# Optimization experiments

Measured on AMD Instinct MI355X. Metric: run time of the kernel, lower is better.

## Reference

```python
import jax, jax.numpy as jnp
import numpy as np

DIM = 1024
HEADS = 16
HEAD_DIM = DIM // HEADS
HIDDEN = 4 * DIM
B, N = 2, 2048
LS_INIT = 1e-4


def _layernorm(x, w, b, eps=1e-5):
    mu = jnp.mean(x, axis=-1, keepdims=True)
    var = jnp.var(x, axis=-1, keepdims=True)
    return (x - mu) * jax.lax.rsqrt(var + eps) * w + b


def setup_inputs() -> dict:
    key = jax.random.key(0)
    ks = jax.random.split(key, 8)
    s = 0.02
    return {
        "x": jax.random.normal(ks[0], (B, N, DIM), jnp.float32),
        "ln1_w": jnp.ones((DIM,), jnp.float32),
        "ln1_b": jnp.zeros((DIM,), jnp.float32),
        "qkv_w": jax.random.normal(ks[1], (3 * DIM, DIM), jnp.float32) * s,
        "qkv_b": jnp.zeros((3 * DIM,), jnp.float32),
        "proj_w": jax.random.normal(ks[2], (DIM, DIM), jnp.float32) * s,
        "proj_b": jnp.zeros((DIM,), jnp.float32),
        "ls1_gamma": jnp.full((DIM,), LS_INIT, jnp.float32),
        "ln2_w": jnp.ones((DIM,), jnp.float32),
        "ln2_b": jnp.zeros((DIM,), jnp.float32),
        "fc1_w": jax.random.normal(ks[3], (HIDDEN, DIM), jnp.float32) * s,
        "fc1_b": jnp.zeros((HIDDEN,), jnp.float32),
        "fc2_w": jax.random.normal(ks[4], (DIM, HIDDEN), jnp.float32) * s,
        "fc2_b": jnp.zeros((DIM,), jnp.float32),
        "ls2_gamma": jnp.full((DIM,), LS_INIT, jnp.float32),
    }


def reference(x, ln1_w, ln1_b, qkv_w, qkv_b, proj_w, proj_b, ls1_gamma,
              ln2_w, ln2_b, fc1_w, fc1_b, fc2_w, fc2_b, ls2_gamma):
    Bn, Nn, C = x.shape
    scale = HEAD_DIM ** -0.5

    # --- attention branch (pre-norm) ---
    h = _layernorm(x, ln1_w, ln1_b)
    qkv = h @ qkv_w.T + qkv_b                      # [B,N,3C]
    qkv = qkv.reshape(Bn, Nn, 3, HEADS, HEAD_DIM)
    q = qkv[:, :, 0].transpose(0, 2, 1, 3)         # [B,H,N,D]
    k = qkv[:, :, 1].transpose(0, 2, 1, 3)
    v = qkv[:, :, 2].transpose(0, 2, 1, 3)
    attn = jnp.einsum('bhnd,bhmd->bhnm', q, k) * scale  # [B,H,N,N]
    attn = jax.nn.softmax(attn, axis=-1)
    o = jnp.einsum('bhnm,bhmd->bhnd', attn, v)
    o = o.transpose(0, 2, 1, 3).reshape(Bn, Nn, C)
    o = o @ proj_w.T + proj_b
    x = x + o * ls1_gamma

    # --- MLP branch (pre-norm) ---
    h = _layernorm(x, ln2_w, ln2_b)
    h = jax.nn.gelu(h @ fc1_w.T + fc1_b, approximate=False)
    h = h @ fc2_w.T + fc2_b
    x = x + h * ls2_gamma
    return x
```

## Files before the change

### kernel.cpp

```cpp
#include <hip/hip_runtime.h>

#define DIM 1024
#define HEADS 16
#define HEAD_DIM 64
#define HIDDEN 4096
#define BB 2
#define NN 2048
#define TOK (BB*NN)

typedef __attribute__((ext_vector_type(8))) short bf16x8;
typedef __attribute__((ext_vector_type(4))) float f32x4;
typedef __attribute__((ext_vector_type(2))) int i32x2;

__device__ inline short f2bf(float f) {
    unsigned u = __float_as_uint(f);
    unsigned r = (u + 0x7fff + ((u >> 16) & 1)) >> 16;
    return (short)r;
}

#define GLL16(g, l)                                                          \
    __builtin_amdgcn_global_load_lds(                                        \
        (const __attribute__((address_space(1))) void*)(g),                  \
        (__attribute__((address_space(3))) void*)(l), 16, 0, 0)

#define BARRIER() do { asm volatile("" ::: "memory");                        \
    __builtin_amdgcn_s_barrier();                                            \
    asm volatile("" ::: "memory"); } while (0)

__global__ void cvt_kernel(const float* __restrict__ in, short* __restrict__ out, int n4) {
    int i = blockIdx.x * blockDim.x + threadIdx.x;
    int stride = gridDim.x * blockDim.x;
    for (; i < n4; i += stride) {
        float4 v = ((const float4*)in)[i];
        short4 o;
        o.x = f2bf(v.x); o.y = f2bf(v.y); o.z = f2bf(v.z); o.w = f2bf(v.w);
        ((short4*)out)[i] = o;
    }
}

__global__ __launch_bounds__(256) void ln_kernel(const float* __restrict__ x,
                                                 const float* __restrict__ w,
                                                 const float* __restrict__ b,
                                                 short* __restrict__ out) {
    const int row = blockIdx.x;
    const int t = threadIdx.x;
    float4 v = ((const float4*)(x + (long)row * DIM))[t];
    float s = v.x + v.y + v.z + v.w;
    float ss = v.x * v.x + v.y * v.y + v.z * v.z + v.w * v.w;
#pragma unroll
    for (int m = 1; m < 64; m <<= 1) {
        s += __shfl_xor(s, m);
        ss += __shfl_xor(ss, m);
    }
    __shared__ float rs[4], rss[4];
    int wv = t >> 6;
    if ((t & 63) == 0) { rs[wv] = s; rss[wv] = ss; }
    __syncthreads();
    s = rs[0] + rs[1] + rs[2] + rs[3];
    ss = rss[0] + rss[1] + rss[2] + rss[3];
    float mean = s * (1.f / DIM);
    float var = ss * (1.f / DIM) - mean * mean;
    float rstd = rsqrtf(var + 1e-5f);
    float4 wv4 = ((const float4*)w)[t];
    float4 bv4 = ((const float4*)b)[t];
    short4 o;
    o.x = f2bf((v.x - mean) * rstd * wv4.x + bv4.x);
    o.y = f2bf((v.y - mean) * rstd * wv4.y + bv4.y);
    o.z = f2bf((v.z - mean) * rstd * wv4.z + bv4.z);
    o.w = f2bf((v.w - mean) * rstd * wv4.w + bv4.w);
    ((short4*)(out + (long)row * DIM))[t] = o;
}

template <int EPI, int BM>
__global__ __launch_bounds__(512, 2) void gemm8(const short* __restrict__ A,
                                                const short* __restrict__ Bt,
                                                const float* __restrict__ bias,
                                                const float* __restrict__ resid,
                                                const float* __restrict__ gamma,
                                                void* __restrict__ Cout,
                                                int M, int N, int K, int nbx) {
    constexpr int ALOADS = BM / 64;
    constexpr int MMP = BM / 64;
    constexpr int AR = BM / 32;

    __shared__ __align__(16) short As[2][BM * 64];
    __shared__ __align__(16) short Bs[2][2][128 * 64];

    const int t = threadIdx.x;
    const int w = t >> 6, l = t & 63, lr = l & 15, lg = l >> 4;
    const int wr = w >> 2, wc = w & 3;

    const int nwg = gridDim.x;
    const int id = blockIdx.x;
    const int r = (id & 7) * (nwg >> 3) + (id >> 3);
    const int by = r / nbx, bx = r % nbx;
    const int rowBase = by * BM, colBase = bx * 256;

    f32x4 acc[AR][4];
#pragma unroll
    for (int m = 0; m < AR; m++)
#pragma unroll
        for (int n = 0; n < 4; n++) acc[m][n] = {0.f, 0.f, 0.f, 0.f};

    bf16x8 afr[MMP][2];
    bf16x8 bfr[4][2];

    const int NT = K >> 6;
    const int ITERS = NT >> 1;

    auto stageA = [&](int buf, int tile) {
        const long k0 = (long)tile * 64;
#pragma unroll
        for (int j = 0; j < ALOADS; j++) {
            int L = j * 512 + t;
            int p = L >> 3;
            int colS = ((L & 7) ^ (p & 7)) << 3;
            const short* g = A + (long)(rowBase + p) * K + k0 + colS;
            GLL16(g, &As[buf][(j * 512 + w * 64) * 8]);
        }
    };
    auto stageBh = [&](int buf, int h, int tile) {
        const long k0 = (long)tile * 64;
#pragma unroll
        for (int j = 0; j < 2; j++) {
            int L = j * 512 + t;
            int p = L >> 3;
            int gcol = ((p >> 5) << 6) + (h << 5) + (p & 31);
            int colS = ((L & 7) ^ (p & 7)) << 3;
            const short* g = Bt + (long)(colBase + gcol) * K + k0 + colS;
            GLL16(g, &Bs[buf][h][(j * 512 + w * 64) * 8]);
        }
    };
    auto ldA = [&](int buf, int mh) {
#pragma unroll
        for (int mm = 0; mm < MMP; mm++) {
            int phys = wr * (BM / 2) + mh * (BM / 4) + mm * 16 + lr;
            int base = phys * 64, sw = (phys & 7) << 3;
#pragma unroll
            for (int ks = 0; ks < 2; ks++)
                afr[mm][ks] = *(const bf16x8*)&As[buf][base + ((ks * 32 + lg * 8) ^ sw)];
        }
    };
    auto ldB = [&](int buf, int nh) {
#pragma unroll
        for (int nn = 0; nn < 2; nn++) {
            int phys = wc * 32 + nn * 16 + lr;
            int base = phys * 64, sw = (phys & 7) << 3;
#pragma unroll
            for (int ks = 0; ks < 2; ks++)
                bfr[nh * 2 + nn][ks] = *(const bf16x8*)&Bs[buf][nh][base + ((ks * 32 + lg * 8) ^ sw)];
        }
    };
    auto mfmaQ = [&](int mh, int nh) {
        __builtin_amdgcn_s_setprio(1);
#pragma unroll
        for (int ks = 0; ks < 2; ks++)
#pragma unroll
            for (int mm = 0; mm < MMP; mm++)
#pragma unroll
                for (int nn = 0; nn < 2; nn++)
                    acc[mh * MMP + mm][nh * 2 + nn] = __builtin_amdgcn_mfma_f32_16x16x32_bf16(
                        afr[mm][ks], bfr[nh * 2 + nn][ks], acc[mh * MMP + mm][nh * 2 + nn], 0, 0, 0);
        __builtin_amdgcn_s_setprio(0);
    };
    auto waitVM = [&]() {
        if constexpr (BM == 256) asm volatile("s_waitcnt vmcnt(8)" ::: "memory");
        else                     asm volatile("s_waitcnt vmcnt(6)" ::: "memory");
    };

    stageBh(0, 0, 0); stageBh(0, 1, 0); stageA(0, 0);
    stageBh(1, 0, 1); stageBh(1, 1, 1); stageA(1, 1);
    waitVM();
    BARRIER();

    for (int i = 0; i < ITERS; i++) {
        const bool more = (i < ITERS - 1);
        ldA(0, 0); ldB(0, 0);
        BARRIER(); mfmaQ(0, 0); BARRIER();
        ldB(0, 1);
        if (more) stageBh(0, 0, 2 * i + 2);
        BARRIER(); mfmaQ(0, 1); BARRIER();
        ldA(0, 1);
        if (more) stageBh(0, 1, 2 * i + 2);
        BARRIER(); mfmaQ(1, 0); BARRIER();
        if (more) { stageA(0, 2 * i + 2); waitVM(); }
        else      { asm volatile("s_waitcnt vmcnt(0)" ::: "memory"); }
        BARRIER(); mfmaQ(1, 1); BARRIER();
        ldA(1, 0); ldB(1, 0);
        BARRIER(); mfmaQ(0, 0); BARRIER();
        ldB(1, 1);
        if (more) stageBh(1, 0, 2 * i + 3);
        BARRIER(); mfmaQ(0, 1); BARRIER();
        ldA(1, 1);
        if (more) stageBh(1, 1, 2 * i + 3);
        BARRIER(); mfmaQ(1, 0); BARRIER();
        if (more) { stageA(1, 2 * i + 3); waitVM(); }
        else      { asm volatile("s_waitcnt vmcnt(0)" ::: "memory"); }
        BARRIER(); mfmaQ(1, 1); BARRIER();
    }

#pragma unroll
    for (int n = 0; n < 4; n++) {
        int col = colBase + wc * 64 + n * 16 + lr;
        float bs = bias[col];
        float gm = (EPI == 3) ? gamma[col] : 0.f;
#pragma unroll
        for (int m = 0; m < AR; m++) {
            int row0 = rowBase + wr * (BM / 2) + m * 16 + lg * 4;
#pragma unroll
            for (int j = 0; j < 4; j++) {
                int row = row0 + j;
                float v = acc[m][n][j] + bs;
                if (EPI == 1) { if (col < DIM) v *= 0.125f; }
                if (EPI == 2) { v = 0.5f * v * (1.f + erff(v * 0.70710678118f)); }
                if (EPI == 3) {
                    float o = resid[(long)row * N + col] + v * gm;
                    ((float*)Cout)[(long)row * N + col] = o;
                } else {
                    ((short*)Cout)[(long)row * N + col] = f2bf(v);
                }
            }
        }
    }
}

__global__ __launch_bounds__(256) void attn_kernel(const short* __restrict__ qkv,
                                                   short* __restrict__ out) {
    const int id = blockIdx.x;
    const int rank = (id & 7) * 128 + (id >> 3);
    const int bh = rank >> 5, qt = rank & 31;
    const int b = bh >> 4, h = bh & 15;
    const int t = threadIdx.x;
    const int w = t >> 6, l = t & 63, lr = l & 15, lg = l >> 4;

    __shared__ __align__(16) short Ks[2][4096];
    __shared__ __align__(16) short Vs[2][4096];
    __shared__ __align__(16) short Ps[4][1024];

    bf16x8 qf[2];
    {
        const int qtok = b * NN + qt * 64 + w * 16 + lr;
        const short* qp = qkv + (long)qtok * (3 * DIM) + h * HEAD_DIM;
        qf[0] = *(const bf16x8*)(qp + lg * 8);
        qf[1] = *(const bf16x8*)(qp + 32 + lg * 8);
    }

    bf16x8 ones;
#pragma unroll
    for (int i = 0; i < 8; i++) ones[i] = (short)0x3F80;

    f32x4 o[4];
#pragma unroll
    for (int dn = 0; dn < 4; dn++) o[dn] = {0.f, 0.f, 0.f, 0.f};
    float mrow[4] = {-1e30f, -1e30f, -1e30f, -1e30f};
    float lrow[4] = {0.f, 0.f, 0.f, 0.f};

    const long tokbase = (long)(b * NN) * (3 * DIM);

    auto stage = [&](int cb, int kv0) {
#pragma unroll
        for (int r = 0; r < 2; r++) {
            int L = r * 256 + t;
            int krow = L >> 3;
            int kcol = ((L & 7) * 8) ^ ((krow & 7) << 3);
            const short* gk = qkv + tokbase + (long)(kv0 + krow) * (3 * DIM) + DIM + h * HEAD_DIM + kcol;
            GLL16(gk, &Ks[cb][(r * 256 + w * 64) * 8]);
            int kv = ((L >> 5) << 2) | ((L >> 1) & 3);
            int d  = ((L >> 3) & 3) * 16 + (L & 1) * 8;
            const short* gv = qkv + tokbase + (long)(kv0 + kv) * (3 * DIM) + 2 * DIM + h * HEAD_DIM + d;
            GLL16(gv, &Vs[cb][(r * 256 + w * 64) * 8]);
        }
    };

    stage(0, 0);
    int cur = 0;

    for (int kvt = 0; kvt < NN / 64; kvt++) {
        __syncthreads();
        if (kvt + 1 < NN / 64) stage(cur ^ 1, (kvt + 1) * 64);

        const int kswz = (lr & 7) << 3;
        f32x4 s[4];
#pragma unroll
        for (int n = 0; n < 4; n++) {
            int rowoff = (n * 16 + lr) * 64;
            bf16x8 kf0 = *(const bf16x8*)&Ks[cur][rowoff + ((lg * 8) ^ kswz)];
            bf16x8 kf1 = *(const bf16x8*)&Ks[cur][rowoff + ((32 + lg * 8) ^ kswz)];
            s[n] = {0.f, 0.f, 0.f, 0.f};
            s[n] = __builtin_amdgcn_mfma_f32_16x16x32_bf16(qf[0], kf0, s[n], 0, 0, 0);
            s[n] = __builtin_amdgcn_mfma_f32_16x16x32_bf16(qf[1], kf1, s[n], 0, 0, 0);
        }

        float corr[4];
#pragma unroll
        for (int j = 0; j < 4; j++) {
            float mx = fmaxf(fmaxf(s[0][j], s[1][j]), fmaxf(s[2][j], s[3][j]));
#pragma unroll
            for (int msk = 1; msk < 16; msk <<= 1) mx = fmaxf(mx, __shfl_xor(mx, msk));
            float mnew = fmaxf(mrow[j], mx);
            corr[j] = __expf(mrow[j] - mnew);
            mrow[j] = mnew;
            int prow = lg * 4 + j;
            int pswz = (prow & 7) << 3;
#pragma unroll
            for (int n = 0; n < 4; n++) {
                float p = __expf(s[n][j] - mnew);
                Ps[w][prow * 64 + ((n * 16 + lr) ^ pswz)] = f2bf(p);
            }
#pragma unroll
            for (int dn = 0; dn < 4; dn++) o[dn][j] *= corr[j];
        }

        i32x2 vrlo[2][4], vrhi[2][4];
#pragma unroll
        for (int kb = 0; kb < 2; kb++)
#pragma unroll
            for (int dn = 0; dn < 4; dn++) {
                unsigned voff = (unsigned)(size_t)&Vs[cur][(kb * 8 + lg * 2) * 256 + dn * 64 + lr];
                asm volatile("ds_read_b64_tr_b16 %0, %2\n\t"
                             "ds_read_b64_tr_b16 %1, %2 offset:512"
                             : "=&v"(vrlo[kb][dn]), "=&v"(vrhi[kb][dn])
                             : "v"(voff));
            }
        asm volatile("s_waitcnt lgkmcnt(0)" ::: "memory");
        __builtin_amdgcn_sched_barrier(0);

        f32x4 lsum = {0.f, 0.f, 0.f, 0.f};
#pragma unroll
        for (int kb = 0; kb < 2; kb++) {
            bf16x8 pf = *(const bf16x8*)&Ps[w][lr * 64 + ((kb * 32 + lg * 8) ^ ((lr & 7) << 3))];
            lsum = __builtin_amdgcn_mfma_f32_16x16x32_bf16(pf, ones, lsum, 0, 0, 0);
#pragma unroll
            for (int dn = 0; dn < 4; dn++) {
                union { i32x2 p[2]; bf16x8 v; } u;
                u.p[0] = vrlo[kb][dn];
                u.p[1] = vrhi[kb][dn];
                o[dn] = __builtin_amdgcn_mfma_f32_16x16x32_bf16(pf, u.v, o[dn], 0, 0, 0);
            }
        }
#pragma unroll
        for (int j = 0; j < 4; j++) lrow[j] = lrow[j] * corr[j] + lsum[j];

        cur ^= 1;
    }

#pragma unroll
    for (int j = 0; j < 4; j++) {
        float inv = 1.f / lrow[j];
        long tok = b * NN + qt * 64 + w * 16 + lg * 4 + j;
#pragma unroll
        for (int dn = 0; dn < 4; dn++)
            out[tok * DIM + h * HEAD_DIM + dn * 16 + lr] = f2bf(o[dn][j] * inv);
    }
}

extern "C" void kernel_launch(void* const* d_in, const int* in_sizes, int n_in,
                              void* d_out, int out_size, void* d_ws, size_t ws_size,
                              hipStream_t stream) {
    const float* x       = (const float*)d_in[0];
    const float* ln1_w   = (const float*)d_in[1];
    const float* ln1_b   = (const float*)d_in[2];
    const float* qkv_w   = (const float*)d_in[3];
    const float* qkv_b   = (const float*)d_in[4];
    const float* proj_w  = (const float*)d_in[5];
    const float* proj_b  = (const float*)d_in[6];
    const float* ls1_g   = (const float*)d_in[7];
    const float* ln2_w   = (const float*)d_in[8];
    const float* ln2_b   = (const float*)d_in[9];
    const float* fc1_w   = (const float*)d_in[10];
    const float* fc1_b   = (const float*)d_in[11];
    const float* fc2_w   = (const float*)d_in[12];
    const float* fc2_b   = (const float*)d_in[13];
    const float* ls2_g   = (const float*)d_in[14];

    char* p = (char*)d_ws;
    short* wqkv   = (short*)p; p += (size_t)3 * DIM * DIM * 2;
    short* wproj  = (short*)p; p += (size_t)DIM * DIM * 2;
    short* wfc1   = (short*)p; p += (size_t)HIDDEN * DIM * 2;
    short* wfc2   = (short*)p; p += (size_t)DIM * HIDDEN * 2;
    short* h1     = (short*)p; p += (size_t)TOK * DIM * 2;
    short* qkvbuf = (short*)p; p += (size_t)TOK * 3 * DIM * 2;
    short* attno  = (short*)p; p += (size_t)TOK * DIM * 2;
    float* x2     = (float*)p; p += (size_t)TOK * DIM * 4;
    short* h2     = (short*)p; p += (size_t)TOK * DIM * 2;
    short* fc1o   = (short*)p; p += (size_t)TOK * HIDDEN * 2;

    {
        int n4;
        n4 = 3 * DIM * DIM / 4;
        cvt_kernel<<<dim3(2048), dim3(256), 0, stream>>>(qkv_w, wqkv, n4);
        n4 = DIM * DIM / 4;
        cvt_kernel<<<dim3(1024), dim3(256), 0, stream>>>(proj_w, wproj, n4);
        n4 = HIDDEN * DIM / 4;
        cvt_kernel<<<dim3(2048), dim3(256), 0, stream>>>(fc1_w, wfc1, n4);
        n4 = DIM * HIDDEN / 4;
        cvt_kernel<<<dim3(2048), dim3(256), 0, stream>>>(fc2_w, wfc2, n4);
    }

    ln_kernel<<<dim3(TOK), dim3(256), 0, stream>>>(x, ln1_w, ln1_b, h1);

    gemm8<1, 256><<<dim3(192), dim3(512), 0, stream>>>(
        h1, wqkv, qkv_b, nullptr, nullptr, qkvbuf, TOK, 3 * DIM, DIM, 12);

    attn_kernel<<<dim3(NN / 64 * BB * HEADS), dim3(256), 0, stream>>>(qkvbuf, attno);

    gemm8<3, 128><<<dim3(128), dim3(512), 0, stream>>>(
        attno, wproj, proj_b, x, ls1_g, x2, TOK, DIM, DIM, 4);

    ln_kernel<<<dim3(TOK), dim3(256), 0, stream>>>(x2, ln2_w, ln2_b, h2);

    gemm8<2, 256><<<dim3(256), dim3(512), 0, stream>>>(
        h2, wfc1, fc1_b, nullptr, nullptr, fc1o, TOK, HIDDEN, DIM, 16);

    gemm8<3, 128><<<dim3(128), dim3(512), 0, stream>>>(
        fc1o, wfc2, fc2_b, x2, ls2_g, (float*)d_out, TOK, DIM, HIDDEN, 4);
}
```

Baseline: 442.8 us.

## Widen attention KV tile to 128 and add lazy softmax rescaling

Doubles the KV tile processed per iteration in the flash-attention kernel from 64 to 128 keys, halving the number of barriers and pipeline stages and enlarging the K/V/P shared buffers. It also skips the running-max update and output rescale unless some lane's new max exceeds the old one by more than 8, a lazy-rescale trick that keeps exp values bounded. V reads are interleaved per k-block rather than loaded all at once. This raises LDS use (about 80KB per block), which may reduce occupancy, and adds register pressure from the 8 score tiles.

```diff
diff --git a/kernel.cpp b/kernel.cpp
--- a/kernel.cpp
+++ b/kernel.cpp
@@ -233,9 +233,9 @@
     const int t = threadIdx.x;
     const int w = t >> 6, l = t & 63, lr = l & 15, lg = l >> 4;
 
-    __shared__ __align__(16) short Ks[2][4096];
-    __shared__ __align__(16) short Vs[2][4096];
-    __shared__ __align__(16) short Ps[4][1024];
+    __shared__ __align__(16) short Ks[2][128 * 64];
+    __shared__ __align__(16) short Vs[2][2 * 4096];
+    __shared__ __align__(16) short Ps[4][16 * 128];
 
     bf16x8 qf[2];
     {
@@ -259,30 +259,35 @@
 
     auto stage = [&](int cb, int kv0) {
 #pragma unroll
-        for (int r = 0; r < 2; r++) {
-            int L = r * 256 + t;
+        for (int j = 0; j < 4; j++) {
+            int L = j * 256 + t;
             int krow = L >> 3;
             int kcol = ((L & 7) * 8) ^ ((krow & 7) << 3);
             const short* gk = qkv + tokbase + (long)(kv0 + krow) * (3 * DIM) + DIM + h * HEAD_DIM + kcol;
-            GLL16(gk, &Ks[cb][(r * 256 + w * 64) * 8]);
-            int kv = ((L >> 5) << 2) | ((L >> 1) & 3);
-            int d  = ((L >> 3) & 3) * 16 + (L & 1) * 8;
-            const short* gv = qkv + tokbase + (long)(kv0 + kv) * (3 * DIM) + 2 * DIM + h * HEAD_DIM + d;
-            GLL16(gv, &Vs[cb][(r * 256 + w * 64) * 8]);
+            GLL16(gk, &Ks[cb][(j * 256 + w * 64) * 8]);
+        }
+#pragma unroll
+        for (int j = 0; j < 4; j++) {
+            int L = j * 256 + t;
+            int hf = L >> 9, Lh = L & 511;
+            int kvl = ((Lh >> 5) << 2) | ((Lh >> 1) & 3);
+            int d  = ((Lh >> 3) & 3) * 16 + (Lh & 1) * 8;
+            const short* gv = qkv + tokbase + (long)(kv0 + hf * 64 + kvl) * (3 * DIM) + 2 * DIM + h * HEAD_DIM + d;
+            GLL16(gv, &Vs[cb][(j * 256 + w * 64) * 8]);
         }
     };
 
     stage(0, 0);
     int cur = 0;
 
-    for (int kvt = 0; kvt < NN / 64; kvt++) {
+    for (int kvt = 0; kvt < NN / 128; kvt++) {
         __syncthreads();
-        if (kvt + 1 < NN / 64) stage(cur ^ 1, (kvt + 1) * 64);
+        if (kvt + 1 < NN / 128) stage(cur ^ 1, (kvt + 1) * 128);
 
         const int kswz = (lr & 7) << 3;
-        f32x4 s[4];
-#pragma unroll
-        for (int n = 0; n < 4; n++) {
+        f32x4 s[8];
+#pragma unroll
+        for (int n = 0; n < 8; n++) {
             int rowoff = (n * 16 + lr) * 64;
             bf16x8 kf0 = *(const bf16x8*)&Ks[cur][rowoff + ((lg * 8) ^ kswz)];
             bf16x8 kf1 = *(const bf16x8*)&Ks[cur][rowoff + ((32 + lg * 8) ^ kswz)];
@@ -294,47 +299,50 @@
         float corr[4];
 #pragma unroll
         for (int j = 0; j < 4; j++) {
-            float mx = fmaxf(fmaxf(s[0][j], s[1][j]), fmaxf(s[2][j], s[3][j]));
+            float mx = s[0][j];
+#pragma unroll
+            for (int n = 1; n < 8; n++) mx = fmaxf(mx, s[n][j]);
 #pragma unroll
             for (int msk = 1; msk < 16; msk <<= 1) mx = fmaxf(mx, __shfl_xor(mx, msk));
-            float mnew = fmaxf(mrow[j], mx);
-            corr[j] = __expf(mrow[j] - mnew);
-            mrow[j] = mnew;
+            corr[j] = 1.f;
+            if (!__all(mx - mrow[j] <= 8.f)) {
+                float mnew = fmaxf(mrow[j], mx);
+                corr[j] = __expf(mrow[j] - mnew);
+                mrow[j] = mnew;
+#pragma unroll
+                for (int dn = 0; dn < 4; dn++) o[dn][j] *= corr[j];
+            }
             int prow = lg * 4 + j;
             int pswz = (prow & 7) << 3;
 #pragma unroll
-            for (int n = 0; n < 4; n++) {
-                float p = __expf(s[n][j] - mnew);
-                Ps[w][prow * 64 + ((n * 16 + lr) ^ pswz)] = f2bf(p);
+            for (int n = 0; n < 8; n++) {
+                float p = __expf(s[n][j] - mrow[j]);
+                Ps[w][prow * 128 + ((n * 16 + lr) ^ pswz)] = f2bf(p);
             }
-#pragma unroll
-            for (int dn = 0; dn < 4; dn++) o[dn][j] *= corr[j];
-        }
-
-        i32x2 vrlo[2][4], vrhi[2][4];
-#pragma unroll
-        for (int kb = 0; kb < 2; kb++)
+        }
+
+        f32x4 lsum = {0.f, 0.f, 0.f, 0.f};
+#pragma unroll
+        for (int kb = 0; kb < 4; kb++) {
+            const int hf = kb >> 1, kb2 = kb & 1;
+            i32x2 vlo[4], vhi[4];
 #pragma unroll
             for (int dn = 0; dn < 4; dn++) {
-                unsigned voff = (unsigned)(size_t)&Vs[cur][(kb * 8 + lg * 2) * 256 + dn * 64 + lr];
+                unsigned voff = (unsigned)(size_t)&Vs[cur][hf * 4096 + (kb2 * 8 + lg * 2) * 256 + dn * 64 + lr];
                 asm volatile("ds_read_b64_tr_b16 %0, %2\n\t"
                              "ds_read_b64_tr_b16 %1, %2 offset:512"
-                             : "=&v"(vrlo[kb][dn]), "=&v"(vrhi[kb][dn])
+                             : "=&v"(vlo[dn]), "=&v"(vhi[dn])
                              : "v"(voff));
             }
-        asm volatile("s_waitcnt lgkmcnt(0)" ::: "memory");
-        __builtin_amdgcn_sched_barrier(0);
-
-        f32x4 lsum = {0.f, 0.f, 0.f, 0.f};
-#pragma unroll
-        for (int kb = 0; kb < 2; kb++) {
-            bf16x8 pf = *(const bf16x8*)&Ps[w][lr * 64 + ((kb * 32 + lg * 8) ^ ((lr & 7) << 3))];
+            bf16x8 pf = *(const bf16x8*)&Ps[w][lr * 128 + ((kb * 32 + lg * 8) ^ ((lr & 7) << 3))];
+            asm volatile("s_waitcnt lgkmcnt(0)" ::: "memory");
+            __builtin_amdgcn_sched_barrier(0);
             lsum = __builtin_amdgcn_mfma_f32_16x16x32_bf16(pf, ones, lsum, 0, 0, 0);
 #pragma unroll
             for (int dn = 0; dn < 4; dn++) {
                 union { i32x2 p[2]; bf16x8 v; } u;
-                u.p[0] = vrlo[kb][dn];
-                u.p[1] = vrhi[kb][dn];
+                u.p[0] = vlo[dn];
+                u.p[1] = vhi[dn];
                 o[dn] = __builtin_amdgcn_mfma_f32_16x16x32_bf16(pf, u.v, o[dn], 0, 0, 0);
             }
         }
```

After: 502.1 us. 1.13x slower.
